# Optimization experiments

Hardware: AMD Instinct MI355X
Metric: run time of the kernel (lower is better)

Reference implementation:

```python
import jax, jax.numpy as jnp
import numpy as np

B, L, D, H, DFF, M = 4, 4096, 1024, 16, 4096, 256
DH = D // H
EPS_LN = 1e-6
EPS_K = 1e-6


def _orthogonal_random_features(m, d, seed=0):
    # Performer create_projection_matrix: stacked orthogonal blocks, rows scaled
    # by chi(d)-distributed norms (scaling=0).
    rng = np.random.RandomState(seed)
    blocks = []
    n_full = m // d
    for _ in range(n_full):
        q, _ = np.linalg.qr(rng.randn(d, d))
        blocks.append(q.T)
    rem = m - n_full * d
    if rem > 0:
        q, _ = np.linalg.qr(rng.randn(d, d))
        blocks.append(q.T[:rem])
    w = np.concatenate(blocks, axis=0)  # [m, d]
    norms = np.linalg.norm(rng.randn(m, d), axis=1, keepdims=True)
    return (norms * w).astype(np.float32)


def setup_inputs() -> dict:
    key = jax.random.key(0)
    ks = jax.random.split(key, 10)
    s = 0.02
    return {
        "x": jax.random.normal(ks[0], (B, L, D), jnp.float32),
        "wq": jax.random.normal(ks[1], (D, H, DH), jnp.float32) * s,
        "wk": jax.random.normal(ks[2], (D, H, DH), jnp.float32) * s,
        "wv": jax.random.normal(ks[3], (D, H, DH), jnp.float32) * s,
        "wo": jax.random.normal(ks[4], (H, DH, D), jnp.float32) * s,
        "proj": jnp.asarray(_orthogonal_random_features(M, DH)),
        "ln1_g": jnp.ones((D,), jnp.float32),
        "ln1_b": jnp.zeros((D,), jnp.float32),
        "ln2_g": jnp.ones((D,), jnp.float32),
        "ln2_b": jnp.zeros((D,), jnp.float32),
        "w1": jax.random.normal(ks[5], (D, DFF), jnp.float32) * s,
        "b1": jnp.zeros((DFF,), jnp.float32),
        "w2": jax.random.normal(ks[6], (DFF, D), jnp.float32) * s,
        "b2": jnp.zeros((D,), jnp.float32),
    }


def _softmax_kernel(data, proj, is_query):
    # FAVOR+ positive softmax feature map. data: [B,L,H,DH], proj: [M,DH]
    dn = 1.0 / jnp.sqrt(jnp.sqrt(jnp.asarray(DH, data.dtype)))
    ratio = 1.0 / jnp.sqrt(jnp.asarray(M, data.dtype))
    dd = jnp.einsum("blhd,md->blhm", data * dn, proj)
    diag = (jnp.sum(jnp.square(data), axis=-1) * (dn * dn) * 0.5)[..., None]  # [B,L,H,1]
    if is_query:
        mx = jnp.max(dd, axis=-1, keepdims=True)
    else:
        mx = jnp.max(dd)
    return ratio * (jnp.exp(dd - diag - mx) + EPS_K)


def _layernorm(x, g, b):
    mu = jnp.mean(x, axis=-1, keepdims=True)
    var = jnp.mean(jnp.square(x - mu), axis=-1, keepdims=True)
    return (x - mu) * jax.lax.rsqrt(var + EPS_LN) * g + b


def reference(x, wq, wk, wv, wo, proj, ln1_g, ln1_b, ln2_g, ln2_b, w1, b1, w2, b2):
    # --- Performer FAVOR+ self-attention (noncausal) ---
    q = jnp.einsum("bld,dhk->blhk", x, wq)
    k = jnp.einsum("bld,dhk->blhk", x, wk)
    v = jnp.einsum("bld,dhk->blhk", x, wv)
    qp = _softmax_kernel(q, proj, True)   # [B,L,H,M]
    kp = _softmax_kernel(k, proj, False)  # [B,L,H,M]
    kv = jnp.einsum("blhm,blhd->bhmd", kp, v)          # [B,H,M,DH]
    num = jnp.einsum("blhm,bhmd->blhd", qp, kv)        # [B,L,H,DH]
    ksum = jnp.sum(kp, axis=1)                          # [B,H,M]
    denom = jnp.einsum("blhm,bhm->blh", qp, ksum)      # [B,L,H]
    attn = num / denom[..., None]
    attn_out = jnp.einsum("blhk,hkd->bld", attn, wo)
    # dropout1 is identity (training=False)
    out1 = _layernorm(x + attn_out, ln1_g, ln1_b)
    # --- FFN ---
    h = jax.nn.elu(jnp.einsum("bld,df->blf", out1, w1) + b1)
    ffn = jnp.einsum("blf,fd->bld", h, w2) + b2
    # dropout2 is identity
    out2 = _layernorm(out1 + ffn, ln2_g, ln2_b)
    return out2
```

## Files before the change

kernel.cpp:

```cpp
#include <hip/hip_runtime.h>

typedef unsigned short ushort_t;
typedef unsigned int uint_t;
typedef __attribute__((ext_vector_type(8))) short s8v;
typedef __attribute__((ext_vector_type(4))) short s4v;
typedef __attribute__((ext_vector_type(4))) float f4v;

#define MFMA(a,b,c) __builtin_amdgcn_mfma_f32_16x16x32_bf16(a,b,c,0,0,0)

#define GLDS16(g, l) \
  __builtin_amdgcn_global_load_lds((const __attribute__((address_space(1))) void*)(g), \
                                   (__attribute__((address_space(3))) void*)(l), 16, 0, 0)

__device__ __forceinline__ float bf2f(short s){
  return __uint_as_float(((uint_t)(ushort_t)s) << 16);
}
__device__ __forceinline__ ushort_t f2bf(float f){
  uint_t u = __float_as_uint(f);
  u += 0x7fffu + ((u >> 16) & 1u);
  return (ushort_t)(u >> 16);
}

__global__ __launch_bounds__(256) void k_cvt_t(const float* __restrict__ src,
    ushort_t* __restrict__ dst, int R, int C){
  __shared__ ushort_t t[64*68];
  const int r0 = blockIdx.x*64, c0 = blockIdx.y*64;
  const int tid = threadIdx.x;
  const int cl = tid>>4, rl4 = (tid&15)*4;
  #pragma unroll
  for(int cc=0; cc<64; cc+=16){
    f4v v = *(const f4v*)(src + (size_t)(c0+cl+cc)*R + r0 + rl4);
    #pragma unroll
    for(int j=0;j<4;j++) t[(rl4+j)*68 + cl+cc] = f2bf(v[j]);
  }
  __syncthreads();
  const int rw = tid>>4, cw4 = (tid&15)*4;
  #pragma unroll
  for(int rr=0; rr<64; rr+=16){
    s4v o;
    #pragma unroll
    for(int j=0;j<4;j++) o[j] = (short)t[(rw+rr)*68 + cw4 + j];
    *(s4v*)(dst + (size_t)(r0+rw+rr)*C + c0 + cw4) = o;
  }
}
__global__ __launch_bounds__(256) void k_proj(const float* __restrict__ src,
    ushort_t* __restrict__ dst){
  int i = blockIdx.x*256 + threadIdx.x;
  if(i < 256*64) dst[i] = f2bf(src[i] * 0.3535533905932738f);
}
__global__ __launch_bounds__(256) void k_f2b4(const float* __restrict__ s,
    ushort_t* __restrict__ d, int n4){
  int i = blockIdx.x*256 + threadIdx.x;
  if(i < n4){
    f4v v = ((const f4v*)s)[i];
    s4v o;
    #pragma unroll
    for(int j=0;j<4;j++) o[j] = (short)f2bf(v[j]);
    ((s4v*)d)[i] = o;
  }
}
__global__ __launch_bounds__(256) void k_zero(float* __restrict__ p, int n){
  int i = blockIdx.x*256 + threadIdx.x;
  if(i < n) p[i] = 0.f;
}

template<int MODE>
__global__ __launch_bounds__(512,2) void gemm8(const ushort_t* __restrict__ A, int lda,
    const ushort_t* __restrict__ Bt, int ldb, ushort_t* __restrict__ Cc, int ldc,
    const float* __restrict__ bias, int M, int N, int K, int G)
{
  __shared__ ushort_t lsh[4][256*64];
  const int tid = threadIdx.x;
  const int wave = tid>>6, lane = tid&63, quad = lane>>4, lid = lane&15;
  const int wm = wave>>2, wn = wave&3;
  const int nwgx = gridDim.x;
  const int nwg  = nwgx * gridDim.y;
  const int orig = blockIdx.y*nwgx + blockIdx.x;
  const int swz  = (orig&7)*(nwg>>3) + (orig>>3);
  const int gsz  = nwgx * G;
  const int g    = swz / gsz;
  const int rem  = swz - g*gsz;
  const int r    = rem / G;
  const int c    = g*G + (rem - r*G);
  const int row0 = r*256, col0 = c*256;

  const int srow = lane>>3;
  const int scol = ((lane&7) ^ srow)*8;
  const ushort_t* gA = A  + (size_t)(row0 + wave*8 + srow)*lda + scol;
  const ushort_t* gB = Bt + (size_t)(col0 + wave*8 + srow)*ldb + scol;
  const int ldsw = wave*512;

  const int aoff = (wm*128 + lid)*64;
  const int boff = (wn*64  + lid)*64;
  const int k0s  = (quad*8)        ^ ((lid&7)<<3);
  const int k1s  = (32 + quad*8)   ^ ((lid&7)<<3);

  f4v acc[8][4];
  #pragma unroll
  for(int m=0;m<8;m++)
    #pragma unroll
    for(int n=0;n<4;n++){ f4v z={0.f,0.f,0.f,0.f}; acc[m][n]=z; }
  s8v af[4][2], bf[4][2];

  const int KT = K>>6;
  const int NP = KT>>1;

#define STG(buf, isB, half, kt) do{ \
    const ushort_t* _g = ((isB)? gB : gA) + (size_t)((half)*128)*((isB)? ldb : lda) + (size_t)(kt)*64; \
    GLDS16(_g, &lsh[(buf)*2+(isB)][(half)*8192 + ldsw]); \
    GLDS16(_g + (size_t)64*((isB)? ldb : lda), &lsh[(buf)*2+(isB)][(half)*8192 + 4096 + ldsw]); \
  }while(0)

#define DSA(buf, mh) do{ \
    const ushort_t* _l = &lsh[(buf)*2][aoff + (mh)*4096]; \
    _Pragma("unroll") \
    for(int _m=0;_m<4;_m++){ \
      af[_m][0] = *(const s8v*)(_l + _m*1024 + k0s); \
      af[_m][1] = *(const s8v*)(_l + _m*1024 + k1s); \
    } \
  }while(0)

#define DSB(buf, nh) do{ \
    const ushort_t* _l = &lsh[(buf)*2+1][boff]; \
    _Pragma("unroll") \
    for(int _n=0;_n<2;_n++){ \
      bf[(nh)*2+_n][0] = *(const s8v*)(_l + ((nh)*2+_n)*1024 + k0s); \
      bf[(nh)*2+_n][1] = *(const s8v*)(_l + ((nh)*2+_n)*1024 + k1s); \
    } \
  }while(0)

#define MMP(mh, nh) do{ \
    __builtin_amdgcn_s_setprio(1); \
    _Pragma("unroll") \
    for(int _m=0;_m<4;_m++) \
      _Pragma("unroll") \
      for(int _n=0;_n<2;_n++){ \
        acc[(mh)*4+_m][(nh)*2+_n] = MFMA(af[_m][0], bf[(nh)*2+_n][0], acc[(mh)*4+_m][(nh)*2+_n]); \
        acc[(mh)*4+_m][(nh)*2+_n] = MFMA(af[_m][1], bf[(nh)*2+_n][1], acc[(mh)*4+_m][(nh)*2+_n]); \
      } \
    __builtin_amdgcn_s_setprio(0); \
  }while(0)

#define BARX  __builtin_amdgcn_s_barrier()
#define LGKM0 do{ asm volatile("s_waitcnt lgkmcnt(0)" ::: "memory"); __builtin_amdgcn_sched_barrier(0); }while(0)
#define VM2   do{ asm volatile("s_waitcnt vmcnt(2)"   ::: "memory"); __builtin_amdgcn_sched_barrier(0); }while(0)

  STG(0,0,0,0); STG(0,0,1,0); STG(0,1,0,0); STG(0,1,1,0);
  STG(1,0,0,1);
  VM2;
  BARX;

  for(int p=0; p<NP; p++){
    const int t1 = 2*p+1;
    const int t2 = (2*p+2 < KT)? 2*p+2 : KT-1;
    const int t3 = (2*p+3 < KT)? 2*p+3 : KT-1;
    DSA(0,0); DSB(0,0); STG(1,0,1,t1);
    asm volatile("s_waitcnt lgkmcnt(8)" ::: "memory");
    BARX; LGKM0; MMP(0,0); BARX;
    DSB(0,1); STG(1,1,0,t1); STG(1,1,1,t1);
    BARX; LGKM0; MMP(0,1); BARX;
    DSA(0,1); STG(0,0,0,t2);
    BARX; LGKM0; MMP(1,0); BARX;
    MMP(1,1); VM2; BARX;
    DSA(1,0); DSB(1,0); STG(0,0,1,t2);
    asm volatile("s_waitcnt lgkmcnt(8)" ::: "memory");
    BARX; LGKM0; MMP(0,0); BARX;
    DSB(1,1); STG(0,1,0,t2); STG(0,1,1,t2);
    BARX; LGKM0; MMP(0,1); BARX;
    DSA(1,1); STG(1,0,0,t3);
    BARX; LGKM0; MMP(1,0); BARX;
    MMP(1,1); VM2; BARX;
  }
  asm volatile("s_waitcnt vmcnt(0)" ::: "memory");

  #pragma unroll
  for(int m=0;m<8;m++){
    const int row = row0 + wm*128 + (m>>2)*64 + (m&3)*16 + quad*4;
    #pragma unroll
    for(int n=0;n<4;n++){
      const int col = col0 + wn*64 + n*16 + lid;
      float bv = 0.f;
      if(MODE>=1) bv = bias[col];
      #pragma unroll
      for(int rr=0;rr<4;rr++){
        float v = acc[m][n][rr] + bv;
        if(MODE==2) v = v>0.f ? v : (__expf(v) - 1.0f);
        Cc[(size_t)(row+rr)*ldc + col] = f2bf(v);
      }
    }
  }
#undef STG
#undef DSA
#undef DSB
#undef MMP
#undef BARX
#undef LGKM0
#undef VM2
}

__global__ __launch_bounds__(256) void k_kv(const ushort_t* __restrict__ qkv,
    const ushort_t* __restrict__ projS,
    float* __restrict__ kvp, float* __restrict__ ksum)
{
  __shared__ ushort_t lK[64*64];
  __shared__ ushort_t lvT[2][64*72];
  __shared__ ushort_t lkp[64*72];
  const int chunk=blockIdx.x, mt=blockIdx.y, bh=blockIdx.z;
  const int h=bh&15, b=bh>>4;
  const int tid=threadIdx.x, wave=tid>>6, lane=tid&63, quad=lane>>4, lid=lane&15;

  s8v pf[4][2];
  {
    const ushort_t* projM = projS + mt*64*64;
    #pragma unroll
    for(int n=0;n<4;n++)
      #pragma unroll
      for(int ks=0;ks<2;ks++)
        pf[n][ks] = *(const s8v*)(projM + (n*16+lid)*64 + ks*32 + quad*8);
  }
  f4v kvacc[4];
  #pragma unroll
  for(int j=0;j<4;j++){ f4v z={0.f,0.f,0.f,0.f}; kvacc[j]=z; }
  float ksacc[4] = {};

  const int sl = tid>>3;
  const int gcb = (tid&7) ^ (sl&7);
  const size_t lbase = (size_t)(b*4096 + chunk*1024);
  const ushort_t* gK0 = qkv + (lbase + sl     )*3072 + 1024 + h*64 + gcb*8;
  const ushort_t* gK1 = qkv + (lbase + sl + 32)*3072 + 1024 + h*64 + gcb*8;
  ushort_t* lK0 = &lK[(wave*8     )*64];
  ushort_t* lK1 = &lK[(wave*8 + 32)*64];
  const ushort_t* gV = qkv + (lbase + lane)*3072 + 2048 + h*64 + wave*16;

  for(int it=0; it<16; it++){
    const int p = it&1;
    GLDS16(gK0, lK0);
    GLDS16(gK1, lK1);
    {
      s8v v0 = *(const s8v*)gV;
      s8v v1 = *(const s8v*)(gV + 8);
      #pragma unroll
      for(int jj=0;jj<8;jj++){
        lvT[p][(wave*16+jj  )*72 + lane] = (ushort_t)v0[jj];
        lvT[p][(wave*16+8+jj)*72 + lane] = (ushort_t)v1[jj];
      }
    }
    gK0 += 64*3072; gK1 += 64*3072; gV += 64*3072;
    __syncthreads();
    float dv;
    {
      const int rl = wave*16 + (lane>>2);
      const int cb0 = 2*(lane&3);
      s8v u0 = *(const s8v*)&lK[rl*64 + ((cb0  )^(rl&7))*8];
      s8v u1 = *(const s8v*)&lK[rl*64 + ((cb0+1)^(rl&7))*8];
      float s = 0.f;
      #pragma unroll
      for(int jj=0;jj<8;jj++){
        float f0=bf2f(u0[jj]), f1=bf2f(u1[jj]);
        s += f0*f0 + f1*f1;
      }
      s += __shfl_xor(s,1,64); s += __shfl_xor(s,2,64);
      dv = s*(1.f/16.f);
    }
    f4v dd[4];
    #pragma unroll
    for(int n=0;n<4;n++){ f4v z={0.f,0.f,0.f,0.f}; dd[n]=z; }
    {
      const int ra = wave*16 + lid;
      #pragma unroll
      for(int ks=0;ks<2;ks++){
        s8v af = *(const s8v*)&lK[ra*64 + ((ks*4+quad)^(ra&7))*8];
        #pragma unroll
        for(int n=0;n<4;n++) dd[n] = MFMA(af, pf[n][ks], dd[n]);
      }
    }
    const int lrb = wave*16 + quad*4;
    #pragma unroll
    for(int n=0;n<4;n++){
      s4v pk;
      #pragma unroll
      for(int r=0;r<4;r++){
        float dg = __shfl(dv, (quad*4+r)*4, 64);
        float ekp = __expf(dd[n][r] - dg) + 1e-6f;
        ksacc[n] += ekp;
        pk[r] = (short)f2bf(ekp);
      }
      *(s4v*)&lkp[(n*16+lid)*72 + lrb] = pk;
    }
    __syncthreads();
    #pragma unroll
    for(int ks=0;ks<2;ks++){
      s8v af = *(const s8v*)&lkp[(wave*16+lid)*72 + ks*32 + quad*8];
      #pragma unroll
      for(int j=0;j<4;j++){
        s8v bfr = *(const s8v*)&lvT[p][(j*16+lid)*72 + ks*32 + quad*8];
        kvacc[j] = MFMA(af, bfr, kvacc[j]);
      }
    }
  }
  #pragma unroll
  for(int n=0;n<4;n++){
    float s = ksacc[n];
    s += __shfl_xor(s,16,64); s += __shfl_xor(s,32,64);
    if(quad==0) atomicAdd(&ksum[((size_t)b*16+h)*256 + mt*64 + n*16 + lid], s);
  }
  float* kvo = kvp + ((size_t)chunk*64 + bh)*16384;
  #pragma unroll
  for(int j=0;j<4;j++)
    #pragma unroll
    for(int r=0;r<4;r++)
      kvo[(mt*64 + wave*16 + quad*4 + r)*64 + j*16 + lid] = kvacc[j][r];
}

__global__ __launch_bounds__(256) void k_f2bt(const float* __restrict__ kvp,
    ushort_t* __restrict__ kvb)
{
  __shared__ ushort_t tb[64*68];
  const int mt=blockIdx.x, bh=blockIdx.y;
  const int tid=threadIdx.x;
  {
    const int ml=tid>>2, dg=(tid&3)*16;
    float s[16];
    #pragma unroll
    for(int e=0;e<16;e++) s[e]=0.f;
    #pragma unroll
    for(int c=0;c<4;c++){
      const float* pb = kvp + ((size_t)(c*64+bh)*256 + mt*64+ml)*64 + dg;
      #pragma unroll
      for(int e4=0;e4<4;e4++){
        f4v v = *(const f4v*)(pb + e4*4);
        #pragma unroll
        for(int j=0;j<4;j++) s[e4*4+j] += v[j];
      }
    }
    #pragma unroll
    for(int e=0;e<16;e++) tb[ml*68 + dg + e] = f2bf(s[e]);
  }
  __syncthreads();
  {
    const int dh=tid>>2, mg=(tid&3)*16;
    ushort_t* ob = kvb + (size_t)bh*16384 + (size_t)dh*256 + mt*64 + mg;
    #pragma unroll
    for(int e4=0;e4<4;e4++){
      s4v o;
      #pragma unroll
      for(int j=0;j<4;j++) o[j] = (short)tb[(mg+e4*4+j)*68 + dh];
      *(s4v*)(ob + e4*4) = o;
    }
  }
}

__global__ __launch_bounds__(256,3) void k_attn(const ushort_t* __restrict__ qkv,
    const ushort_t* __restrict__ projS, const ushort_t* __restrict__ kvT,
    const float* __restrict__ ksum, ushort_t* __restrict__ attnW)
{
  __shared__ ushort_t lkv[64*256];
  __shared__ ushort_t lqp[64*136];
  const int lt=blockIdx.x, h=blockIdx.y, b=blockIdx.z;
  const int tid=threadIdx.x, wave=tid>>6, lane=tid&63, quad=lane>>4, lid=lane&15;
  const ushort_t* kvbG = kvT + ((size_t)b*16+h)*(64*256);
  const float* ksb = ksum + ((size_t)b*16+h)*256;
  float kse[16];
  #pragma unroll
  for(int n=0;n<16;n++) kse[n] = ksb[n*16+lid];
  const int sdh = tid>>5;
  const int scb = tid&31;

  #pragma unroll
  for(int t=0;t<2;t++){
    const int l0 = lt*128 + t*64;
    const ushort_t* qbase = qkv + (size_t)(b*4096+l0+wave*16+lid)*3072 + h*64;
    const s8v af0 = *(const s8v*)(qbase + quad*8);
    const s8v af1 = *(const s8v*)(qbase + 32 + quad*8);
    f4v num[4];
    #pragma unroll
    for(int j=0;j<4;j++){ f4v z={0.f,0.f,0.f,0.f}; num[j]=z; }
    float dnm[4] = {0.f,0.f,0.f,0.f};

    #pragma unroll
    for(int mc=0; mc<2; mc++){
      f4v dd[8];
      #pragma unroll
      for(int n=0;n<8;n++){ f4v z={0.f,0.f,0.f,0.f}; dd[n]=z; }
      #pragma unroll
      for(int n=0;n<8;n++){
        const ushort_t* pb = projS + ((mc*8+n)*16+lid)*64 + quad*8;
        s8v b0 = *(const s8v*)(pb);
        s8v b1 = *(const s8v*)(pb + 32);
        dd[n] = MFMA(af0, b0, dd[n]);
        dd[n] = MFMA(af1, b1, dd[n]);
      }
      if(t==0 && mc==0){
        __builtin_amdgcn_sched_barrier(0);
        #pragma unroll
        for(int q=0;q<8;q++){
          const int dh = q*8 + sdh;
          GLDS16(kvbG + dh*256 + ((scb ^ (dh&7))*8),
                 &lkv[(size_t)(q*8 + wave*2)*256]);
        }
        __builtin_amdgcn_sched_barrier(0);
      }
      #pragma unroll
      for(int r=0;r<4;r++){
        const int lrow = wave*16 + quad*4 + r;
        #pragma unroll
        for(int n=0;n<8;n++){
          float e = __expf(dd[n][r]) + 1e-6f;
          dnm[r] += e * kse[mc*8+n];
          lqp[lrow*136 + n*16 + lid] = f2bf(e);
        }
      }
      if(t==0 && mc==0){
        asm volatile("s_waitcnt vmcnt(0)" ::: "memory");
        __syncthreads();
      } else {
        asm volatile("s_waitcnt lgkmcnt(0)" ::: "memory");
        __builtin_amdgcn_sched_barrier(0);
      }
      #pragma unroll
      for(int ks=0;ks<4;ks++){
        s8v a = *(const s8v*)&lqp[(wave*16+lid)*136 + ks*32 + quad*8];
        #pragma unroll
        for(int j=0;j<4;j++){
          const int cbr = mc*16 + ks*4 + quad;
          s8v bfr = *(const s8v*)&lkv[(size_t)(j*16+lid)*256 + ((cbr ^ (lid&7))*8)];
          num[j] = MFMA(a, bfr, num[j]);
        }
      }
      asm volatile("s_waitcnt lgkmcnt(0)" ::: "memory");
      __builtin_amdgcn_sched_barrier(0);
    }
    #pragma unroll
    for(int r=0;r<4;r++){
      float s = dnm[r];
      s += __shfl_xor(s,1,64); s += __shfl_xor(s,2,64);
      s += __shfl_xor(s,4,64); s += __shfl_xor(s,8,64);
      dnm[r] = s;
    }
    #pragma unroll
    for(int j=0;j<4;j++)
      #pragma unroll
      for(int r=0;r<4;r++){
        const int row = b*4096 + l0 + wave*16 + quad*4 + r;
        attnW[(size_t)row*3072 + h*64 + j*16 + lid] = f2bf(num[j][r] / dnm[r]);
      }
  }
}

template<int FINAL>
__global__ __launch_bounds__(256) void k_ln(const float* __restrict__ xres,
    const ushort_t* __restrict__ aa, int lda_a,
    const ushort_t* __restrict__ bbf, int lda_b,
    const float* __restrict__ g, const float* __restrict__ be,
    ushort_t* __restrict__ obf, int ldo, float* __restrict__ of)
{
  const int w = threadIdx.x>>6, lane = threadIdx.x&63;
  const int row = blockIdx.x*4 + w;
  float v[16];
  #pragma unroll
  for(int k=0;k<4;k++){
    const int c = lane*4 + k*256;
    if(FINAL==0){
      f4v xv = *(const f4v*)(xres + (size_t)row*1024 + c);
      s4v av = *(const s4v*)(aa + (size_t)row*lda_a + c);
      #pragma unroll
      for(int j=0;j<4;j++) v[k*4+j] = xv[j] + bf2f(av[j]);
    } else {
      s4v av = *(const s4v*)(aa + (size_t)row*lda_a + c);
      s4v bv = *(const s4v*)(bbf + (size_t)row*lda_b + c);
      #pragma unroll
      for(int j=0;j<4;j++) v[k*4+j] = bf2f(av[j]) + bf2f(bv[j]);
    }
  }
  float s = 0.f;
  #pragma unroll
  for(int e=0;e<16;e++) s += v[e];
  #pragma unroll
  for(int o=1;o<64;o<<=1) s += __shfl_xor(s, o, 64);
  const float mu = s * (1.f/1024.f);
  float q = 0.f;
  #pragma unroll
  for(int e=0;e<16;e++){ float d=v[e]-mu; q += d*d; }
  #pragma unroll
  for(int o=1;o<64;o<<=1) q += __shfl_xor(q, o, 64);
  const float rs = rsqrtf(q*(1.f/1024.f) + 1e-6f);
  #pragma unroll
  for(int k=0;k<4;k++){
    const int c = lane*4 + k*256;
    f4v gv = *(const f4v*)(g + c);
    f4v bev = *(const f4v*)(be + c);
    if(FINAL==0){
      s4v o;
      #pragma unroll
      for(int j=0;j<4;j++) o[j] = (short)f2bf((v[k*4+j]-mu)*rs*gv[j] + bev[j]);
      *(s4v*)(obf + (size_t)row*ldo + c) = o;
    } else {
      f4v o;
      #pragma unroll
      for(int j=0;j<4;j++) o[j] = (v[k*4+j]-mu)*rs*gv[j] + bev[j];
      *(f4v*)(of + (size_t)row*1024 + c) = o;
    }
  }
}

extern "C" void kernel_launch(void* const* d_in, const int* in_sizes, int n_in,
                              void* d_out, int out_size, void* d_ws, size_t ws_size,
                              hipStream_t stream) {
  (void)in_sizes; (void)n_in; (void)out_size;
  const float* x    = (const float*)d_in[0];
  const float* wq   = (const float*)d_in[1];
  const float* wk   = (const float*)d_in[2];
  const float* wv   = (const float*)d_in[3];
  const float* wo   = (const float*)d_in[4];
  const float* proj = (const float*)d_in[5];
  const float* ln1g = (const float*)d_in[6];
  const float* ln1b = (const float*)d_in[7];
  const float* ln2g = (const float*)d_in[8];
  const float* ln2b = (const float*)d_in[9];
  const float* w1   = (const float*)d_in[10];
  const float* b1   = (const float*)d_in[11];
  const float* w2   = (const float*)d_in[12];
  const float* b2   = (const float*)d_in[13];

  char* wsb = (char*)d_ws;
  size_t off = 0;
  auto alloc = [&](size_t bytes)->char*{
    char* p = wsb + off; off = (off + bytes + 255) & ~(size_t)255; return p;
  };
  ushort_t* wqkvT = (ushort_t*)alloc(3072ull*1024*2);
  ushort_t* woT   = (ushort_t*)alloc(1024ull*1024*2);
  ushort_t* w1T   = (ushort_t*)alloc(4096ull*1024*2);
  ushort_t* w2T   = (ushort_t*)alloc(1024ull*4096*2);
  ushort_t* projS = (ushort_t*)alloc(256*64*2);
  ushort_t* qkv   = (ushort_t*)alloc(16384ull*3072*2);
  size_t zoff = off;
  float*    ksumb = (float*)alloc(4ull*16*256*4);
  size_t zlen = off - zoff;
  ushort_t* kvb   = (ushort_t*)alloc(4ull*16*64*256*2);

  const size_t hbBytes = 16384ull*4096*2;
  ushort_t* hbWS = nullptr;
  if(off + hbBytes <= ws_size) hbWS = (ushort_t*)alloc(hbBytes);

  ushort_t* out1 = qkv;
  ushort_t* ao   = qkv + 1024;
  ushort_t* attn = qkv + 2048;
  ushort_t* ffn  = qkv + 2048;
  ushort_t* xb   = (ushort_t*)d_out;
  float*    kvp  = (float*)d_out;

  k_cvt_t<<<dim3(16,16),256,0,stream>>>(wq, wqkvT,                1024, 1024);
  k_cvt_t<<<dim3(16,16),256,0,stream>>>(wk, wqkvT + 1024ull*1024, 1024, 1024);
  k_cvt_t<<<dim3(16,16),256,0,stream>>>(wv, wqkvT + 2048ull*1024, 1024, 1024);
  k_cvt_t<<<dim3(16,16),256,0,stream>>>(wo, woT, 1024, 1024);
  k_cvt_t<<<dim3(64,16),256,0,stream>>>(w1, w1T, 4096, 1024);
  k_cvt_t<<<dim3(16,64),256,0,stream>>>(w2, w2T, 1024, 4096);
  k_proj<<<64,256,0,stream>>>(proj, projS);
  k_f2b4<<<16384,256,0,stream>>>(x, xb, 16384*1024/4);
  {
    int nz = (int)(zlen/4);
    k_zero<<<(nz+255)/256,256,0,stream>>>((float*)(wsb+zoff), nz);
  }

  gemm8<0><<<dim3(64,12),512,0,stream>>>(xb, 1024, wqkvT, 1024, qkv, 3072, nullptr, 16384, 3072, 1024, 4);
  k_kv<<<dim3(4,4,64),256,0,stream>>>(qkv, projS, kvp, ksumb);
  k_f2bt<<<dim3(4,64),256,0,stream>>>(kvp, kvb);
  k_attn<<<dim3(32,16,4),256,0,stream>>>(qkv, projS, kvb, ksumb, attn);
  gemm8<0><<<dim3(64,4),512,0,stream>>>(attn, 3072, woT, 1024, ao, 3072, nullptr, 16384, 1024, 1024, 4);
  k_ln<0><<<4096,256,0,stream>>>(x, ao, 3072, nullptr, 0, ln1g, ln1b, out1, 3072, nullptr);
  if(hbWS){
    gemm8<2><<<dim3(64,16),512,0,stream>>>(out1, 3072, w1T, 1024, hbWS, 4096, b1, 16384, 4096, 1024, 8);
    gemm8<1><<<dim3(64,4),512,0,stream>>>(hbWS, 4096, w2T, 4096, ffn, 3072, b2, 16384, 1024, 4096, 4);
  } else {
    ushort_t* hb = (ushort_t*)d_out;
    for(int c=0;c<2;c++){
      const size_t ro = (size_t)c*8192*3072;
      gemm8<2><<<dim3(32,16),512,0,stream>>>(out1 + ro, 3072, w1T, 1024, hb, 4096, b1, 8192, 4096, 1024, 8);
      gemm8<1><<<dim3(32,4),512,0,stream>>>(hb, 4096, w2T, 4096, ffn + ro, 3072, b2, 8192, 1024, 4096, 4);
    }
  }
  k_ln<1><<<4096,256,0,stream>>>(nullptr, out1, 3072, ffn, 3072, ln2g, ln2b, nullptr, 0, (float*)d_out);
}
```

Measured before the change: 733.8 us.

## Vectorize GEMM epilogue stores and replace ksum atomics with partial buffers

The GEMM epilogue now transposes each 4x4 accumulator fragment with lane shuffles, so each lane writes four contiguous bf16 values as one 8-byte store instead of four scattered 2-byte stores. The ksum reduction in k_kv writes per-chunk, per-wave partials instead of using atomicAdd; k_attn sums the 16 partials itself, which also removes the zero-fill kernel. The four 1024x1024 weight transposes are merged into one launch, and the x conversion uses a grid-stride loop with fewer blocks. In exchange the epilogue does extra shuffles, and each k_attn block reads 16 partial values per ksum entry.

```diff
diff --git a/kernel.cpp b/kernel.cpp
--- a/kernel.cpp
+++ b/kernel.cpp
@@ -5,6 +5,7 @@
 typedef __attribute__((ext_vector_type(8))) short s8v;
 typedef __attribute__((ext_vector_type(4))) short s4v;
 typedef __attribute__((ext_vector_type(4))) float f4v;
+typedef __attribute__((ext_vector_type(2))) unsigned int u2v;
 
 #define MFMA(a,b,c) __builtin_amdgcn_mfma_f32_16x16x32_bf16(a,b,c,0,0,0)
 
@@ -21,6 +22,30 @@
   return (ushort_t)(u >> 16);
 }
 
+struct Cvt4Args { const float* s[4]; ushort_t* d[4]; };
+__global__ __launch_bounds__(256) void k_cvt4(Cvt4Args a){
+  __shared__ ushort_t t[64*68];
+  const float* src = a.s[blockIdx.z];
+  ushort_t* dst = a.d[blockIdx.z];
+  const int r0 = blockIdx.x*64, c0 = blockIdx.y*64;
+  const int tid = threadIdx.x;
+  const int cl = tid>>4, rl4 = (tid&15)*4;
+  #pragma unroll
+  for(int cc=0; cc<64; cc+=16){
+    f4v v = *(const f4v*)(src + (size_t)(c0+cl+cc)*1024 + r0 + rl4);
+    #pragma unroll
+    for(int j=0;j<4;j++) t[(rl4+j)*68 + cl+cc] = f2bf(v[j]);
+  }
+  __syncthreads();
+  const int rw = tid>>4, cw4 = (tid&15)*4;
+  #pragma unroll
+  for(int rr=0; rr<64; rr+=16){
+    s4v o;
+    #pragma unroll
+    for(int j=0;j<4;j++) o[j] = (short)t[(rw+rr)*68 + cw4 + j];
+    *(s4v*)(dst + (size_t)(r0+rw+rr)*1024 + c0 + cw4) = o;
+  }
+}
 __global__ __launch_bounds__(256) void k_cvt_t(const float* __restrict__ src,
     ushort_t* __restrict__ dst, int R, int C){
   __shared__ ushort_t t[64*68];
@@ -50,18 +75,13 @@
 }
 __global__ __launch_bounds__(256) void k_f2b4(const float* __restrict__ s,
     ushort_t* __restrict__ d, int n4){
-  int i = blockIdx.x*256 + threadIdx.x;
-  if(i < n4){
+  for(int i = blockIdx.x*256 + threadIdx.x; i < n4; i += gridDim.x*256){
     f4v v = ((const f4v*)s)[i];
     s4v o;
     #pragma unroll
     for(int j=0;j<4;j++) o[j] = (short)f2bf(v[j]);
     ((s4v*)d)[i] = o;
   }
-}
-__global__ __launch_bounds__(256) void k_zero(float* __restrict__ p, int n){
-  int i = blockIdx.x*256 + threadIdx.x;
-  if(i < n) p[i] = 0.f;
 }
 
 template<int MODE>
@@ -173,20 +193,32 @@
   }
   asm volatile("s_waitcnt vmcnt(0)" ::: "memory");
 
-  #pragma unroll
-  for(int m=0;m<8;m++){
-    const int row = row0 + wm*128 + (m>>2)*64 + (m&3)*16 + quad*4;
-    #pragma unroll
-    for(int n=0;n<4;n++){
-      const int col = col0 + wn*64 + n*16 + lid;
-      float bv = 0.f;
-      if(MODE>=1) bv = bias[col];
-      #pragma unroll
-      for(int rr=0;rr<4;rr++){
-        float v = acc[m][n][rr] + bv;
-        if(MODE==2) v = v>0.f ? v : (__expf(v) - 1.0f);
-        Cc[(size_t)(row+rr)*ldc + col] = f2bf(v);
-      }
+  const int s0 = lane&1, s1 = lane&2;
+  #pragma unroll
+  for(int n=0;n<4;n++){
+    f4v bv4 = {0.f,0.f,0.f,0.f};
+    const int col = col0 + wn*64 + n*16 + (lid&12);
+    if(MODE>=1) bv4 = *(const f4v*)&bias[col];
+    #pragma unroll
+    for(int m=0;m<8;m++){
+      float a0=acc[m][n][0], a1=acc[m][n][1], a2=acc[m][n][2], a3=acc[m][n][3];
+      float t;
+      t = __shfl_xor(s0 ? a0 : a1, 1, 64); a0 = s0 ? t : a0; a1 = s0 ? a1 : t;
+      t = __shfl_xor(s0 ? a2 : a3, 1, 64); a2 = s0 ? t : a2; a3 = s0 ? a3 : t;
+      t = __shfl_xor(s1 ? a0 : a2, 2, 64); a0 = s1 ? t : a0; a2 = s1 ? a2 : t;
+      t = __shfl_xor(s1 ? a1 : a3, 2, 64); a1 = s1 ? t : a1; a3 = s1 ? a3 : t;
+      a0 += bv4[0]; a1 += bv4[1]; a2 += bv4[2]; a3 += bv4[3];
+      if(MODE==2){
+        a0 = a0>0.f ? a0 : (__expf(a0)-1.f);
+        a1 = a1>0.f ? a1 : (__expf(a1)-1.f);
+        a2 = a2>0.f ? a2 : (__expf(a2)-1.f);
+        a3 = a3>0.f ? a3 : (__expf(a3)-1.f);
+      }
+      u2v o;
+      o[0] = ((uint_t)f2bf(a1)<<16) | (uint_t)f2bf(a0);
+      o[1] = ((uint_t)f2bf(a3)<<16) | (uint_t)f2bf(a2);
+      const int row = row0 + wm*128 + (m>>2)*64 + (m&3)*16 + quad*4 + (lid&3);
+      *(u2v*)(Cc + (size_t)row*ldc + col) = o;
     }
   }
 #undef STG
@@ -200,7 +232,7 @@
 
 __global__ __launch_bounds__(256) void k_kv(const ushort_t* __restrict__ qkv,
     const ushort_t* __restrict__ projS,
-    float* __restrict__ kvp, float* __restrict__ ksum)
+    float* __restrict__ kvp, float* __restrict__ ksump)
 {
   __shared__ ushort_t lK[64*64];
   __shared__ ushort_t lvT[2][64*72];
@@ -302,7 +334,8 @@
   for(int n=0;n<4;n++){
     float s = ksacc[n];
     s += __shfl_xor(s,16,64); s += __shfl_xor(s,32,64);
-    if(quad==0) atomicAdd(&ksum[((size_t)b*16+h)*256 + mt*64 + n*16 + lid], s);
+    if(quad==0)
+      ksump[(((size_t)chunk*4 + wave)*64 + bh)*256 + mt*64 + n*16 + lid] = s;
   }
   float* kvo = kvp + ((size_t)chunk*64 + bh)*16384;
   #pragma unroll
@@ -352,17 +385,23 @@
 
 __global__ __launch_bounds__(256,3) void k_attn(const ushort_t* __restrict__ qkv,
     const ushort_t* __restrict__ projS, const ushort_t* __restrict__ kvT,
-    const float* __restrict__ ksum, ushort_t* __restrict__ attnW)
+    const float* __restrict__ ksump, ushort_t* __restrict__ attnW)
 {
   __shared__ ushort_t lkv[64*256];
   __shared__ ushort_t lqp[64*136];
   const int lt=blockIdx.x, h=blockIdx.y, b=blockIdx.z;
   const int tid=threadIdx.x, wave=tid>>6, lane=tid&63, quad=lane>>4, lid=lane&15;
-  const ushort_t* kvbG = kvT + ((size_t)b*16+h)*(64*256);
-  const float* ksb = ksum + ((size_t)b*16+h)*256;
+  const int bh = b*16 + h;
+  const ushort_t* kvbG = kvT + ((size_t)bh)*(64*256);
   float kse[16];
   #pragma unroll
-  for(int n=0;n<16;n++) kse[n] = ksb[n*16+lid];
+  for(int n=0;n<16;n++){
+    float s = 0.f;
+    #pragma unroll
+    for(int sl=0;sl<16;sl++)
+      s += ksump[((size_t)sl*64 + bh)*256 + n*16 + lid];
+    kse[n] = s;
+  }
   const int sdh = tid>>5;
   const int scb = tid&31;
 
@@ -533,9 +572,7 @@
   ushort_t* w2T   = (ushort_t*)alloc(1024ull*4096*2);
   ushort_t* projS = (ushort_t*)alloc(256*64*2);
   ushort_t* qkv   = (ushort_t*)alloc(16384ull*3072*2);
-  size_t zoff = off;
-  float*    ksumb = (float*)alloc(4ull*16*256*4);
-  size_t zlen = off - zoff;
+  float*    ksump = (float*)alloc(16ull*64*256*4);
   ushort_t* kvb   = (ushort_t*)alloc(4ull*16*64*256*2);
 
   const size_t hbBytes = 16384ull*4096*2;
@@ -549,23 +586,21 @@
   ushort_t* xb   = (ushort_t*)d_out;
   float*    kvp  = (float*)d_out;
 
-  k_cvt_t<<<dim3(16,16),256,0,stream>>>(wq, wqkvT,                1024, 1024);
-  k_cvt_t<<<dim3(16,16),256,0,stream>>>(wk, wqkvT + 1024ull*1024, 1024, 1024);
-  k_cvt_t<<<dim3(16,16),256,0,stream>>>(wv, wqkvT + 2048ull*1024, 1024, 1024);
-  k_cvt_t<<<dim3(16,16),256,0,stream>>>(wo, woT, 1024, 1024);
+  {
+    Cvt4Args ca;
+    ca.s[0]=wq; ca.s[1]=wk; ca.s[2]=wv; ca.s[3]=wo;
+    ca.d[0]=wqkvT; ca.d[1]=wqkvT+1024ull*1024; ca.d[2]=wqkvT+2048ull*1024; ca.d[3]=woT;
+    k_cvt4<<<dim3(16,16,4),256,0,stream>>>(ca);
+  }
   k_cvt_t<<<dim3(64,16),256,0,stream>>>(w1, w1T, 4096, 1024);
   k_cvt_t<<<dim3(16,64),256,0,stream>>>(w2, w2T, 1024, 4096);
   k_proj<<<64,256,0,stream>>>(proj, projS);
-  k_f2b4<<<16384,256,0,stream>>>(x, xb, 16384*1024/4);
-  {
-    int nz = (int)(zlen/4);
-    k_zero<<<(nz+255)/256,256,0,stream>>>((float*)(wsb+zoff), nz);
-  }
+  k_f2b4<<<2048,256,0,stream>>>(x, xb, 16384*1024/4);
 
   gemm8<0><<<dim3(64,12),512,0,stream>>>(xb, 1024, wqkvT, 1024, qkv, 3072, nullptr, 16384, 3072, 1024, 4);
-  k_kv<<<dim3(4,4,64),256,0,stream>>>(qkv, projS, kvp, ksumb);
+  k_kv<<<dim3(4,4,64),256,0,stream>>>(qkv, projS, kvp, ksump);
   k_f2bt<<<dim3(4,64),256,0,stream>>>(kvp, kvb);
-  k_attn<<<dim3(32,16,4),256,0,stream>>>(qkv, projS, kvb, ksumb, attn);
+  k_attn<<<dim3(32,16,4),256,0,stream>>>(qkv, projS, kvb, ksump, attn);
   gemm8<0><<<dim3(64,4),512,0,stream>>>(attn, 3072, woT, 1024, ao, 3072, nullptr, 16384, 1024, 1024, 4);
   k_ln<0><<<4096,256,0,stream>>>(x, ao, 3072, nullptr, 0, ln1g, ln1b, out1, 3072, nullptr);
   if(hbWS){
```

Result: slower. 857.0 us (+16.8%).
